# Kernel tuning notes

Hardware: AMD Instinct MI355X
Metric: run time of the kernel (lower is better)

## Reference

```python
import jax, jax.numpy as jnp
import numpy as np

B, C, T = 8, 512, 4096          # batch, channels (query/key/value/calc), time
NUM_HEADS = 8
HEAD_DIM = C // NUM_HEADS
EPS = 1e-6


def _rmsnorm(x, g):
    # x: [B, C, T], normalize over channel dim (num_features)
    return x * jax.lax.rsqrt(jnp.mean(x * x, axis=1, keepdims=True) + EPS) * g[None, :, None]


def _conv1x1(x, W, b):
    # pointwise Conv1d: W [out, in], x [B, in, T]
    return jnp.einsum('oc,bct->bot', W, x) + b[None, :, None]


def _feature(x, W, b, g):
    # Conv1d -> RMSNorm -> elu(x)+1
    return jax.nn.elu(_rmsnorm(_conv1x1(x, W, b), g)) + 1.0


def setup_inputs() -> dict:
    key = jax.random.key(0)
    ks = jax.random.split(key, 16)
    s = 1.0 / np.sqrt(C)
    inp = {
        'queries': jax.random.normal(ks[0], (B, C, T), dtype=jnp.float32),
        'keys': jax.random.normal(ks[1], (B, C, T), dtype=jnp.float32),
        'values': jax.random.normal(ks[2], (B, C, T), dtype=jnp.float32),
        'key_padding_masks': jax.random.randint(ks[3], (B, T), 0, 2).astype(bool),
        'Wq': jax.random.normal(ks[4], (C, C), dtype=jnp.float32) * s,
        'bq': jnp.zeros((C,), dtype=jnp.float32),
        'gq': jnp.ones((C,), dtype=jnp.float32),
        'Wk': jax.random.normal(ks[5], (C, C), dtype=jnp.float32) * s,
        'bk': jnp.zeros((C,), dtype=jnp.float32),
        'gk': jnp.ones((C,), dtype=jnp.float32),
        'Wv': jax.random.normal(ks[6], (C, C), dtype=jnp.float32) * s,
        'bv': jnp.zeros((C,), dtype=jnp.float32),
        'gv': jnp.ones((C,), dtype=jnp.float32),
        'Wp': jax.random.normal(ks[7], (C, C), dtype=jnp.float32) * s,
        'bp': jnp.zeros((C,), dtype=jnp.float32),
        'g_out': jnp.ones((C,), dtype=jnp.float32),
    }
    return inp


def reference(queries, keys, values, key_padding_masks,
              Wq, bq, gq, Wk, bk, gk, Wv, bv, gv, Wp, bp, g_out):
    residuals = queries
    q = _feature(queries, Wq, bq, gq)   # [B, C, Tq]
    k = _feature(keys, Wk, bk, gk)      # [B, C, Tk]
    v = _feature(values, Wv, bv, gv)    # [B, C, Tk]

    # split heads: (head dim) channel layout -> [B, H, Dh, T]
    q = q.reshape(B, NUM_HEADS, HEAD_DIM, -1)
    k = k.reshape(B, NUM_HEADS, HEAD_DIM, -1)
    v = v.reshape(B, NUM_HEADS, HEAD_DIM, -1)

    k = jnp.where(key_padding_masks[:, None, None, :], -10000.0, k)

    q = jax.nn.softmax(q, axis=2) * (NUM_HEADS ** -0.5)  # softmax over head_dim
    k = jax.nn.softmax(k, axis=3)                         # softmax over key time
    v = v / HEAD_DIM

    # linear attention: KV composition then QKV
    ctx = jnp.einsum('bhkt,bhvt->bhkv', k, v)             # [B, H, Dh, Dh]
    out = jnp.einsum('bhqt,bhqv->bhvt', q, ctx)           # [B, H, Dh, Tq]

    out = out.reshape(B, C, -1)
    out = _conv1x1(out, Wp, bp)
    return _rmsnorm(out + residuals, g_out)
```

## Files before the change

### kernel.cpp

```cpp
#include <hip/hip_runtime.h>
#include <hip/hip_bf16.h>

#define BB 8
#define CC 512
#define TT 4096
#define HH 8
#define DH 64
#define EPS 1e-6f

#define NROWS (BB * TT)

using bf16x8 = __attribute__((ext_vector_type(8))) short;
using s16x4  = __attribute__((ext_vector_type(4))) short;
using f32x4  = __attribute__((ext_vector_type(4))) float;

__device__ __forceinline__ short f2b(float f) {
  __hip_bfloat16 h = __float2bfloat16(f);
  return *reinterpret_cast<short*>(&h);
}
__device__ __forceinline__ float b2f(short s) {
  unsigned u = ((unsigned)(unsigned short)s) << 16;
  return __uint_as_float(u);
}

__device__ __forceinline__ void gld16(short* lds_dst, const short* gsrc) {
  __builtin_amdgcn_global_load_lds(
      (const __attribute__((address_space(1))) unsigned int*)gsrc,
      (__attribute__((address_space(3))) unsigned int*)lds_dst, 16, 0, 0);
}

__global__ __launch_bounds__(256) void conv_w4(const float* __restrict__ s0, const float* __restrict__ s1,
                                               const float* __restrict__ s2, const float* __restrict__ s3,
                                               short* __restrict__ d0, short* __restrict__ d1,
                                               short* __restrict__ d2, short* __restrict__ d3)
{
  const float* src; short* dst;
  switch (blockIdx.y) {
    case 0: src = s0; dst = d0; break;
    case 1: src = s1; dst = d1; break;
    case 2: src = s2; dst = d2; break;
    default: src = s3; dst = d3; break;
  }
  int i8 = (blockIdx.x * 256 + threadIdx.x) * 8;
  float4 a = *(const float4*)(src + i8);
  float4 b = *(const float4*)(src + i8 + 4);
  bf16x8 h = { f2b(a.x), f2b(a.y), f2b(a.z), f2b(a.w),
               f2b(b.x), f2b(b.y), f2b(b.z), f2b(b.w) };
  *(bf16x8*)(dst + i8) = h;
}

__global__ __launch_bounds__(256) void transpose_cvt3(const float* __restrict__ X0,
                                                      const float* __restrict__ X1,
                                                      const float* __restrict__ X2,
                                                      short* __restrict__ Y0,
                                                      short* __restrict__ Y1,
                                                      short* __restrict__ Y2)
{
  __shared__ short tile[64 * 68];
  const int t0 = blockIdx.x * 64, c0 = blockIdx.y * 64;
  const int b = blockIdx.z & 7, which = blockIdx.z >> 3;
  const float* X = which == 0 ? X0 : (which == 1 ? X1 : X2);
  short* Xt = which == 0 ? Y0 : (which == 1 ? Y1 : Y2);
  const int tid = threadIdx.x;
  {
    int cl = tid >> 4, t4 = (tid & 15) * 4;
    #pragma unroll
    for (int it = 0; it < 4; ++it) {
      int c = it * 16 + cl;
      float4 v = *(const float4*)(X + ((size_t)b * CC + c0 + c) * TT + t0 + t4);
      s16x4 h = { f2b(v.x), f2b(v.y), f2b(v.z), f2b(v.w) };
      *(s16x4*)&tile[c * 68 + t4] = h;
    }
  }
  __syncthreads();
  {
    int t = tid >> 2, ci = (tid & 3) * 16;
    short s[16];
    #pragma unroll
    for (int i = 0; i < 16; ++i) s[i] = tile[(ci + i) * 68 + t];
    short* dst = Xt + ((size_t)b * TT + t0 + t) * CC + c0 + ci;
    *(bf16x8*)dst = *(bf16x8*)&s[0];
    *(bf16x8*)(dst + 8) = *(bf16x8*)&s[8];
  }
}

__global__ __launch_bounds__(256) void gemm_tc(const short* __restrict__ A,
                                               const short* __restrict__ W,
                                               const float* __restrict__ bias,
                                               short* __restrict__ Y)
{
  __shared__ short As[2][4096];
  __shared__ short Bs[2][4096];
  const int tid = threadIdx.x;
  int x = blockIdx.x;
  int wg = (x & 7) * 128 + (x >> 3);
  const int m0 = (wg >> 2) * 128;
  const int o0 = (wg & 3) * 128;

  const int wid = tid >> 6, lane = tid & 63;
  const int wr = (wid >> 1) * 64, wc = (wid & 1) * 64;
  const int lr = lane & 15, g = lane >> 4;
  const int swz8 = (g ^ ((lr >> 1) & 3)) * 8;

  const int srow0 = tid >> 2;
  const int scol  = ((tid & 3) ^ ((tid >> 3) & 3)) * 8;

  f32x4 acc[4][4] = {};

  #pragma unroll
  for (int it = 0; it < 2; ++it) {
    int row = it * 64 + srow0;
    gld16(&As[0][it * 2048 + tid * 8], A + (size_t)(m0 + row) * CC + scol);
    gld16(&Bs[0][it * 2048 + tid * 8], W + (size_t)(o0 + row) * CC + scol);
  }
  __syncthreads();

  for (int step = 0; step < 16; ++step) {
    const int cur = step & 1;
    if (step < 15) {
      const int k0 = (step + 1) * 32;
      #pragma unroll
      for (int it = 0; it < 2; ++it) {
        int row = it * 64 + srow0;
        gld16(&As[cur ^ 1][it * 2048 + tid * 8], A + (size_t)(m0 + row) * CC + k0 + scol);
        gld16(&Bs[cur ^ 1][it * 2048 + tid * 8], W + (size_t)(o0 + row) * CC + k0 + scol);
      }
    }
    bf16x8 af[4], bf[4];
    #pragma unroll
    for (int m = 0; m < 4; ++m) af[m] = *(const bf16x8*)&As[cur][(wr + m * 16 + lr) * 32 + swz8];
    #pragma unroll
    for (int n = 0; n < 4; ++n) bf[n] = *(const bf16x8*)&Bs[cur][(wc + n * 16 + lr) * 32 + swz8];
    #pragma unroll
    for (int m = 0; m < 4; ++m)
      #pragma unroll
      for (int n = 0; n < 4; ++n)
        acc[m][n] = __builtin_amdgcn_mfma_f32_16x16x32_bf16(af[m], bf[n], acc[m][n], 0, 0, 0);
    __syncthreads();
  }

  const int lq4 = (lane >> 4) * 4;
  #pragma unroll
  for (int m = 0; m < 4; ++m)
    #pragma unroll
    for (int r = 0; r < 4; ++r) {
      size_t row = (size_t)(m0 + wr + m * 16 + lq4 + r) * CC;
      #pragma unroll
      for (int n = 0; n < 4; ++n) {
        int o = o0 + wc + n * 16 + lr;
        Y[row + o] = f2b(acc[m][n][r] + bias[o]);
      }
    }
}

template<int MODE>
__global__ __launch_bounds__(256) void feat_row(short* __restrict__ buf,
                                                const float* __restrict__ g,
                                                const unsigned char* __restrict__ mask)
{
  const int row = blockIdx.x * 4 + (threadIdx.x >> 6);
  const int lane = threadIdx.x & 63;
  short* p = buf + (size_t)row * CC + lane * 8;
  if constexpr (MODE == 1) {
    if (mask[row]) {
      bf16x8 z = { 0,0,0,0,0,0,0,0 };
      *(bf16x8*)p = z;
      return;
    }
  }
  bf16x8 v = *(const bf16x8*)p;
  float x[8], ss = 0.f;
  #pragma unroll
  for (int j = 0; j < 8; ++j) { x[j] = b2f(v[j]); ss += x[j] * x[j]; }
  #pragma unroll
  for (int off = 32; off; off >>= 1) ss += __shfl_xor(ss, off);
  float rn = rsqrtf(ss * (1.0f / CC) + EPS);
  float4 g0 = *(const float4*)(g + lane * 8);
  float4 g1 = *(const float4*)(g + lane * 8 + 4);
  float gv[8] = { g0.x, g0.y, g0.z, g0.w, g1.x, g1.y, g1.z, g1.w };
  float f[8];
  #pragma unroll
  for (int j = 0; j < 8; ++j) {
    float t = x[j] * rn * gv[j];
    f[j] = t > 0.f ? t + 1.f : __expf(t);
  }
  bf16x8 o;
  if constexpr (MODE == 1) {
    #pragma unroll
    for (int j = 0; j < 8; ++j) o[j] = f2b(__expf(f[j]));
  } else if constexpr (MODE == 2) {
    #pragma unroll
    for (int j = 0; j < 8; ++j) o[j] = f2b(f[j] * (1.0f / DH));
  } else {
    float ls = 0.f;
    #pragma unroll
    for (int j = 0; j < 8; ++j) { f[j] = __expf(f[j]); ls += f[j]; }
    ls += __shfl_xor(ls, 1); ls += __shfl_xor(ls, 2); ls += __shfl_xor(ls, 4);
    float sc = 0.35355339059327373f / ls;
    #pragma unroll
    for (int j = 0; j < 8; ++j) o[j] = f2b(f[j] * sc);
  }
  *(bf16x8*)p = o;
}

__global__ __launch_bounds__(256) void ksm_sum(const short* __restrict__ kfe,
                                               float* __restrict__ S)
{
  const int b = blockIdx.y, tch = blockIdx.x;
  const int c2 = threadIdx.x * 2;
  float s0 = 0.f, s1 = 0.f;
  for (int t = 0; t < 128; ++t) {
    unsigned u = *(const unsigned*)&kfe[((size_t)b * TT + tch * 128 + t) * CC + c2];
    s0 += __uint_as_float(u << 16);
    s1 += __uint_as_float(u & 0xffff0000u);
  }
  atomicAdd(&S[b * CC + c2], s0);
  atomicAdd(&S[b * CC + c2 + 1], s1);
}

__global__ __launch_bounds__(256) void ctx_t(const short* __restrict__ kf,
                                             const short* __restrict__ vf,
                                             float* __restrict__ P)
{
  __shared__ short Ks[64 * 64];
  __shared__ short Vs[64 * 64];
  const int tc = blockIdx.x, bh = blockIdx.y;
  const int b = bh >> 3, h = bh & 7;
  const int tid = threadIdx.x, wid = tid >> 6, lane = tid & 63;
  const int lr = lane & 15, lg = lane >> 4;
  f32x4 acc[4] = {};

  for (int ts = 0; ts < 8; ++ts) {
    #pragma unroll
    for (int i = 0; i < 2; ++i) {
      int n = i * 256 + tid;
      int t = n >> 3, ch = (n & 7) * 8;
      size_t src = ((size_t)b * TT + tc * 512 + ts * 64 + t) * CC + h * DH + ch;
      gld16(Ks + n * 8, kf + src);
      gld16(Vs + n * 8, vf + src);
    }
    __syncthreads();
    #pragma unroll
    for (int kk = 0; kk < 64; kk += 32) {
      short a[8];
      #pragma unroll
      for (int j = 0; j < 8; ++j)
        a[j] = Ks[(kk + lg * 8 + j) * 64 + wid * 16 + lr];
      bf16x8 af = *(const bf16x8*)&a[0];
      #pragma unroll
      for (int n = 0; n < 4; ++n) {
        short bv[8];
        #pragma unroll
        for (int j = 0; j < 8; ++j)
          bv[j] = Vs[(kk + lg * 8 + j) * 64 + n * 16 + lr];
        acc[n] = __builtin_amdgcn_mfma_f32_16x16x32_bf16(af, *(const bf16x8*)&bv[0],
                                                         acc[n], 0, 0, 0);
      }
    }
    __syncthreads();
  }
  float* pp = P + ((size_t)tc * 64 + bh) * (DH * DH);
  const int lq4 = lg * 4;
  #pragma unroll
  for (int n = 0; n < 4; ++n)
    #pragma unroll
    for (int r = 0; r < 4; ++r)
      pp[(wid * 16 + lq4 + r) * DH + n * 16 + lr] = acc[n][r];
}

__global__ __launch_bounds__(256) void ctx_reduce(const float* __restrict__ P,
                                                  const float* __restrict__ S,
                                                  short* __restrict__ CT)
{
  int i = blockIdx.x * 256 + threadIdx.x;
  float s = 0.f;
  #pragma unroll
  for (int c = 0; c < 8; ++c) s += P[(size_t)c * 64 * DH * DH + i];
  int bh = i >> 12, rem = i & 4095, q = rem >> 6, v = rem & 63;
  int b = bh >> 3, h = bh & 7;
  float inv = 1.f / S[b * CC + h * DH + q];
  CT[((size_t)bh << 12) + v * 64 + q] = f2b(s * inv);
}

__global__ __launch_bounds__(256) void attn_t(const short* __restrict__ qf,
                                              const short* __restrict__ CT,
                                              short* __restrict__ ao)
{
  __shared__ short As[128 * 72];
  __shared__ short Cs[64 * 72];
  const int m0 = blockIdx.x * 128, h = blockIdx.y;
  const int tid = threadIdx.x, wid = tid >> 6, lane = tid & 63;
  const int lr = lane & 15, lk8 = (lane >> 4) * 8;

  #pragma unroll
  for (int i = 0; i < 4; ++i) {
    int n = i * 256 + tid;
    int r = n >> 3, ch = (n & 7) * 8;
    *(bf16x8*)&As[r * 72 + ch] =
        *(const bf16x8*)(qf + (size_t)(m0 + r) * CC + h * DH + ch);
  }
  {
    const int bh0 = (m0 / TT) * 8 + h;
    #pragma unroll
    for (int i = 0; i < 2; ++i) {
      int n = i * 256 + tid;
      int v = n >> 3, ch = (n & 7) * 8;
      *(bf16x8*)&Cs[v * 72 + ch] = *(const bf16x8*)(CT + ((size_t)bh0 << 12) + v * 64 + ch);
    }
  }
  __syncthreads();

  const int wr = wid * 32;
  f32x4 acc[2][4] = {};
  #pragma unroll
  for (int kk = 0; kk < 64; kk += 32) {
    bf16x8 af[2], cf[4];
    #pragma unroll
    for (int m = 0; m < 2; ++m) af[m] = *(const bf16x8*)&As[(wr + m * 16 + lr) * 72 + kk + lk8];
    #pragma unroll
    for (int n = 0; n < 4; ++n) cf[n] = *(const bf16x8*)&Cs[(n * 16 + lr) * 72 + kk + lk8];
    #pragma unroll
    for (int m = 0; m < 2; ++m)
      #pragma unroll
      for (int n = 0; n < 4; ++n)
        acc[m][n] = __builtin_amdgcn_mfma_f32_16x16x32_bf16(af[m], cf[n], acc[m][n], 0, 0, 0);
  }
  const int lq4 = (lane >> 4) * 4;
  #pragma unroll
  for (int m = 0; m < 2; ++m)
    #pragma unroll
    for (int r = 0; r < 4; ++r) {
      size_t row = (size_t)(m0 + wr + m * 16 + lq4 + r) * CC + h * DH;
      #pragma unroll
      for (int n = 0; n < 4; ++n)
        ao[row + n * 16 + lr] = f2b(acc[m][n][r]);
    }
}

__global__ __launch_bounds__(256) void final_fused(const short* __restrict__ pj,
                                                   const short* __restrict__ qt,
                                                   const float* __restrict__ g,
                                                   float* __restrict__ out)
{
  __shared__ float tile[64 * 65];
  __shared__ float rmss[64];
  const int t0 = blockIdx.x * 64, b = blockIdx.y;
  const int tid = threadIdx.x;

  {
    const int t = tid >> 2, cb = (tid & 3) * 128;
    const size_t row = ((size_t)b * TT + t0 + t) * CC + cb;
    float ss = 0.f;
    #pragma unroll
    for (int j = 0; j < 16; ++j) {
      bf16x8 a = *(const bf16x8*)(pj + row + j * 8);
      bf16x8 q = *(const bf16x8*)(qt + row + j * 8);
      #pragma unroll
      for (int e = 0; e < 8; ++e) { float z = b2f(a[e]) + b2f(q[e]); ss += z * z; }
    }
    ss += __shfl_xor(ss, 1);
    ss += __shfl_xor(ss, 2);
    if ((tid & 3) == 0) rmss[t] = rsqrtf(ss * (1.0f / CC) + EPS);
  }
  __syncthreads();

  for (int cb8 = 0; cb8 < 8; ++cb8) {
    const int c0 = cb8 * 64;
    {
      const int t = tid >> 2, ch = (tid & 3) * 16;
      const size_t row = ((size_t)b * TT + t0 + t) * CC + c0 + ch;
      bf16x8 a0 = *(const bf16x8*)(pj + row);
      bf16x8 a1 = *(const bf16x8*)(pj + row + 8);
      bf16x8 q0 = *(const bf16x8*)(qt + row);
      bf16x8 q1 = *(const bf16x8*)(qt + row + 8);
      const float r = rmss[t];
      #pragma unroll
      for (int j = 0; j < 8; ++j) {
        tile[(ch + j) * 65 + t]     = (b2f(a0[j]) + b2f(q0[j])) * r * g[c0 + ch + j];
        tile[(ch + 8 + j) * 65 + t] = (b2f(a1[j]) + b2f(q1[j])) * r * g[c0 + ch + 8 + j];
      }
    }
    __syncthreads();
    {
      const int c = tid >> 2, tc = (tid & 3) * 16;
      float* dst = out + ((size_t)b * CC + c0 + c) * TT + t0 + tc;
      #pragma unroll
      for (int i = 0; i < 4; ++i) {
        float4 v = { tile[c * 65 + tc + i * 4],     tile[c * 65 + tc + i * 4 + 1],
                     tile[c * 65 + tc + i * 4 + 2], tile[c * 65 + tc + i * 4 + 3] };
        *(float4*)(dst + i * 4) = v;
      }
    }
    __syncthreads();
  }
}

extern "C" void kernel_launch(void* const* d_in, const int* in_sizes, int n_in,
                              void* d_out, int out_size, void* d_ws, size_t ws_size,
                              hipStream_t stream) {
  (void)in_sizes; (void)n_in; (void)out_size; (void)ws_size;
  const float* queries = (const float*)d_in[0];
  const float* keys    = (const float*)d_in[1];
  const float* values  = (const float*)d_in[2];
  const unsigned char* mask = (const unsigned char*)d_in[3];
  const float* Wq = (const float*)d_in[4];
  const float* bq = (const float*)d_in[5];
  const float* gq = (const float*)d_in[6];
  const float* Wk = (const float*)d_in[7];
  const float* bk = (const float*)d_in[8];
  const float* gk = (const float*)d_in[9];
  const float* Wv = (const float*)d_in[10];
  const float* bv = (const float*)d_in[11];
  const float* gv = (const float*)d_in[12];
  const float* Wp = (const float*)d_in[13];
  const float* bp = (const float*)d_in[14];
  const float* g_out = (const float*)d_in[15];

  const size_t NCT = (size_t)NROWS * CC;
  short* qt = (short*)d_ws;
  short* kt = qt + NCT;
  short* vt = kt + NCT;
  short* qf = vt + NCT;
  short* kf = qf + NCT;
  short* vf = kf + NCT;
  short* ao = kt;
  short* pj = vt;
  float* ctxP = (float*)(vf + NCT);
  short* CT  = (short*)(ctxP + (size_t)8 * 64 * DH * DH);
  short* wqb = CT + (size_t)64 * DH * DH;
  short* wkb = wqb + (size_t)CC * CC;
  short* wvb = wkb + (size_t)CC * CC;
  short* wpb = wvb + (size_t)CC * CC;
  float* S   = (float*)(wpb + (size_t)CC * CC);

  hipMemsetAsync(S, 0, (size_t)BB * CC * sizeof(float), stream);

  conv_w4<<<dim3(CC * CC / 2048, 4), 256, 0, stream>>>(Wq, Wk, Wv, Wp, wqb, wkb, wvb, wpb);

  transpose_cvt3<<<dim3(TT / 64, CC / 64, 3 * BB), 256, 0, stream>>>(
      queries, keys, values, qt, kt, vt);

  dim3 gG(1024);
  gemm_tc<<<gG, 256, 0, stream>>>(qt, wqb, bq, qf);
  gemm_tc<<<gG, 256, 0, stream>>>(kt, wkb, bk, kf);
  gemm_tc<<<gG, 256, 0, stream>>>(vt, wvb, bv, vf);

  feat_row<0><<<dim3(NROWS / 4), 256, 0, stream>>>(qf, gq, mask);
  feat_row<1><<<dim3(NROWS / 4), 256, 0, stream>>>(kf, gk, mask);
  feat_row<2><<<dim3(NROWS / 4), 256, 0, stream>>>(vf, gv, mask);

  ksm_sum<<<dim3(32, BB), 256, 0, stream>>>(kf, S);

  ctx_t<<<dim3(8, BB * HH), 256, 0, stream>>>(kf, vf, ctxP);
  ctx_reduce<<<dim3(64 * DH * DH / 256), 256, 0, stream>>>(ctxP, S, CT);

  attn_t<<<dim3(NROWS / 128, HH), 256, 0, stream>>>(qf, CT, ao);

  gemm_tc<<<gG, 256, 0, stream>>>(ao, wpb, bp, pj);

  final_fused<<<dim3(TT / 64, BB), 256, 0, stream>>>(pj, qt, g_out, (float*)d_out);
}
```

Before: 339.9 us.

## Batch QKV GEMMs and feature kernels, pipeline transpose, cache residual in LDS

Merges the three QKV projection GEMMs and the three feature-normalization kernels into single launches indexed by blockIdx.y. The transpose kernel now processes four 64-wide time tiles per block, prefetching the next tile into registers while double-buffering LDS. The final RMSNorm kernel keeps the bf16 residual sum in a large LDS buffer so the projection and residual are read from global memory only once. This trades launch count and global traffic for much higher LDS use per block, which lowers occupancy, and adds bf16 rounding of the residual sum before the final scale.

```diff
diff --git a/kernel.cpp b/kernel.cpp
--- a/kernel.cpp
+++ b/kernel.cpp
@@ -56,32 +56,124 @@
                                                       short* __restrict__ Y1,
                                                       short* __restrict__ Y2)
 {
-  __shared__ short tile[64 * 68];
-  const int t0 = blockIdx.x * 64, c0 = blockIdx.y * 64;
+  __shared__ short tile[2][64 * 68];
+  const int t0 = blockIdx.x * 256, c0 = blockIdx.y * 64;
   const int b = blockIdx.z & 7, which = blockIdx.z >> 3;
   const float* X = which == 0 ? X0 : (which == 1 ? X1 : X2);
   short* Xt = which == 0 ? Y0 : (which == 1 ? Y1 : Y2);
   const int tid = threadIdx.x;
-  {
-    int cl = tid >> 4, t4 = (tid & 15) * 4;
+  const int cl = tid >> 4, t4 = (tid & 15) * 4;
+  const int tb = tid >> 2, ci = (tid & 3) * 16;
+
+  float4 r[4];
+  #pragma unroll
+  for (int it = 0; it < 4; ++it)
+    r[it] = *(const float4*)(X + ((size_t)b * CC + c0 + it * 16 + cl) * TT + t0 + t4);
+
+  for (int s = 0; s < 4; ++s) {
+    const int cur = s & 1;
     #pragma unroll
     for (int it = 0; it < 4; ++it) {
-      int c = it * 16 + cl;
-      float4 v = *(const float4*)(X + ((size_t)b * CC + c0 + c) * TT + t0 + t4);
-      s16x4 h = { f2b(v.x), f2b(v.y), f2b(v.z), f2b(v.w) };
-      *(s16x4*)&tile[c * 68 + t4] = h;
-    }
+      s16x4 h = { f2b(r[it].x), f2b(r[it].y), f2b(r[it].z), f2b(r[it].w) };
+      *(s16x4*)&tile[cur][(it * 16 + cl) * 68 + t4] = h;
+    }
+    if (s < 3) {
+      #pragma unroll
+      for (int it = 0; it < 4; ++it)
+        r[it] = *(const float4*)(X + ((size_t)b * CC + c0 + it * 16 + cl) * TT
+                                 + t0 + (s + 1) * 64 + t4);
+    }
+    __syncthreads();
+    short sreg[16];
+    #pragma unroll
+    for (int i = 0; i < 16; ++i) sreg[i] = tile[cur][(ci + i) * 68 + tb];
+    short* dst = Xt + ((size_t)b * TT + t0 + s * 64 + tb) * CC + c0 + ci;
+    *(bf16x8*)dst = *(bf16x8*)&sreg[0];
+    *(bf16x8*)(dst + 8) = *(bf16x8*)&sreg[8];
+  }
+}
+
+__device__ __forceinline__ void gemm_body(const short* __restrict__ A,
+                                          const short* __restrict__ W,
+                                          const float* __restrict__ bias,
+                                          short* __restrict__ Y,
+                                          short* As, short* Bs, int x, int tid)
+{
+  int wg = (x & 7) * 128 + (x >> 3);
+  const int m0 = (wg >> 2) * 128;
+  const int o0 = (wg & 3) * 128;
+
+  const int wid = tid >> 6, lane = tid & 63;
+  const int wr = (wid >> 1) * 64, wc = (wid & 1) * 64;
+  const int lr = lane & 15, g = lane >> 4;
+  const int swz8 = (g ^ ((lr >> 1) & 3)) * 8;
+
+  const int srow0 = tid >> 2;
+  const int scol  = ((tid & 3) ^ ((tid >> 3) & 3)) * 8;
+
+  f32x4 acc[4][4] = {};
+
+  #pragma unroll
+  for (int it = 0; it < 2; ++it) {
+    int row = it * 64 + srow0;
+    gld16(&As[it * 2048 + tid * 8], A + (size_t)(m0 + row) * CC + scol);
+    gld16(&Bs[it * 2048 + tid * 8], W + (size_t)(o0 + row) * CC + scol);
   }
   __syncthreads();
-  {
-    int t = tid >> 2, ci = (tid & 3) * 16;
-    short s[16];
-    #pragma unroll
-    for (int i = 0; i < 16; ++i) s[i] = tile[(ci + i) * 68 + t];
-    short* dst = Xt + ((size_t)b * TT + t0 + t) * CC + c0 + ci;
-    *(bf16x8*)dst = *(bf16x8*)&s[0];
-    *(bf16x8*)(dst + 8) = *(bf16x8*)&s[8];
-  }
+
+  for (int step = 0; step < 16; ++step) {
+    const int cur = step & 1;
+    if (step < 15) {
+      const int k0 = (step + 1) * 32;
+      #pragma unroll
+      for (int it = 0; it < 2; ++it) {
+        int row = it * 64 + srow0;
+        gld16(&As[(cur ^ 1) * 4096 + it * 2048 + tid * 8], A + (size_t)(m0 + row) * CC + k0 + scol);
+        gld16(&Bs[(cur ^ 1) * 4096 + it * 2048 + tid * 8], W + (size_t)(o0 + row) * CC + k0 + scol);
+      }
+    }
+    bf16x8 af[4], bf[4];
+    #pragma unroll
+    for (int m = 0; m < 4; ++m) af[m] = *(const bf16x8*)&As[cur * 4096 + (wr + m * 16 + lr) * 32 + swz8];
+    #pragma unroll
+    for (int n = 0; n < 4; ++n) bf[n] = *(const bf16x8*)&Bs[cur * 4096 + (wc + n * 16 + lr) * 32 + swz8];
+    #pragma unroll
+    for (int m = 0; m < 4; ++m)
+      #pragma unroll
+      for (int n = 0; n < 4; ++n)
+        acc[m][n] = __builtin_amdgcn_mfma_f32_16x16x32_bf16(af[m], bf[n], acc[m][n], 0, 0, 0);
+    __syncthreads();
+  }
+
+  const int lq4 = (lane >> 4) * 4;
+  #pragma unroll
+  for (int m = 0; m < 4; ++m)
+    #pragma unroll
+    for (int r = 0; r < 4; ++r) {
+      size_t row = (size_t)(m0 + wr + m * 16 + lq4 + r) * CC;
+      #pragma unroll
+      for (int n = 0; n < 4; ++n) {
+        int o = o0 + wc + n * 16 + lr;
+        Y[row + o] = f2b(acc[m][n][r] + bias[o]);
+      }
+    }
+}
+
+__global__ __launch_bounds__(256) void gemm_tc3(
+    const short* __restrict__ A0, const short* __restrict__ A1, const short* __restrict__ A2,
+    const short* __restrict__ W0, const short* __restrict__ W1, const short* __restrict__ W2,
+    const float* __restrict__ b0, const float* __restrict__ b1, const float* __restrict__ b2,
+    short* __restrict__ Y0, short* __restrict__ Y1, short* __restrict__ Y2)
+{
+  __shared__ short As[2 * 4096];
+  __shared__ short Bs[2 * 4096];
+  const short *A, *W; const float* bias; short* Y;
+  switch (blockIdx.y) {
+    case 0:  A = A0; W = W0; bias = b0; Y = Y0; break;
+    case 1:  A = A1; W = W1; bias = b1; Y = Y1; break;
+    default: A = A2; W = W2; bias = b2; Y = Y2; break;
+  }
+  gemm_body(A, W, bias, Y, As, Bs, blockIdx.x, threadIdx.x);
 }
 
 __global__ __launch_bounds__(256) void gemm_tc(const short* __restrict__ A,
@@ -89,84 +181,28 @@
                                                const float* __restrict__ bias,
                                                short* __restrict__ Y)
 {
-  __shared__ short As[2][4096];
-  __shared__ short Bs[2][4096];
-  const int tid = threadIdx.x;
-  int x = blockIdx.x;
-  int wg = (x & 7) * 128 + (x >> 3);
-  const int m0 = (wg >> 2) * 128;
-  const int o0 = (wg & 3) * 128;
-
-  const int wid = tid >> 6, lane = tid & 63;
-  const int wr = (wid >> 1) * 64, wc = (wid & 1) * 64;
-  const int lr = lane & 15, g = lane >> 4;
-  const int swz8 = (g ^ ((lr >> 1) & 3)) * 8;
-
-  const int srow0 = tid >> 2;
-  const int scol  = ((tid & 3) ^ ((tid >> 3) & 3)) * 8;
-
-  f32x4 acc[4][4] = {};
-
-  #pragma unroll
-  for (int it = 0; it < 2; ++it) {
-    int row = it * 64 + srow0;
-    gld16(&As[0][it * 2048 + tid * 8], A + (size_t)(m0 + row) * CC + scol);
-    gld16(&Bs[0][it * 2048 + tid * 8], W + (size_t)(o0 + row) * CC + scol);
-  }
-  __syncthreads();
-
-  for (int step = 0; step < 16; ++step) {
-    const int cur = step & 1;
-    if (step < 15) {
-      const int k0 = (step + 1) * 32;
-      #pragma unroll
-      for (int it = 0; it < 2; ++it) {
-        int row = it * 64 + srow0;
-        gld16(&As[cur ^ 1][it * 2048 + tid * 8], A + (size_t)(m0 + row) * CC + k0 + scol);
-        gld16(&Bs[cur ^ 1][it * 2048 + tid * 8], W + (size_t)(o0 + row) * CC + k0 + scol);
-      }
-    }
-    bf16x8 af[4], bf[4];
-    #pragma unroll
-    for (int m = 0; m < 4; ++m) af[m] = *(const bf16x8*)&As[cur][(wr + m * 16 + lr) * 32 + swz8];
-    #pragma unroll
-    for (int n = 0; n < 4; ++n) bf[n] = *(const bf16x8*)&Bs[cur][(wc + n * 16 + lr) * 32 + swz8];
-    #pragma unroll
-    for (int m = 0; m < 4; ++m)
-      #pragma unroll
-      for (int n = 0; n < 4; ++n)
-        acc[m][n] = __builtin_amdgcn_mfma_f32_16x16x32_bf16(af[m], bf[n], acc[m][n], 0, 0, 0);
-    __syncthreads();
-  }
-
-  const int lq4 = (lane >> 4) * 4;
-  #pragma unroll
-  for (int m = 0; m < 4; ++m)
-    #pragma unroll
-    for (int r = 0; r < 4; ++r) {
-      size_t row = (size_t)(m0 + wr + m * 16 + lq4 + r) * CC;
-      #pragma unroll
-      for (int n = 0; n < 4; ++n) {
-        int o = o0 + wc + n * 16 + lr;
-        Y[row + o] = f2b(acc[m][n][r] + bias[o]);
-      }
-    }
-}
-
-template<int MODE>
-__global__ __launch_bounds__(256) void feat_row(short* __restrict__ buf,
-                                                const float* __restrict__ g,
+  __shared__ short As[2 * 4096];
+  __shared__ short Bs[2 * 4096];
+  gemm_body(A, W, bias, Y, As, Bs, blockIdx.x, threadIdx.x);
+}
+
+__global__ __launch_bounds__(256) void feat_all(short* __restrict__ qf, short* __restrict__ kf,
+                                                short* __restrict__ vf,
+                                                const float* __restrict__ gq,
+                                                const float* __restrict__ gk,
+                                                const float* __restrict__ gv,
                                                 const unsigned char* __restrict__ mask)
 {
+  const int mode = blockIdx.y;
+  short* buf = mode == 0 ? qf : (mode == 1 ? kf : vf);
+  const float* g = mode == 0 ? gq : (mode == 1 ? gk : gv);
   const int row = blockIdx.x * 4 + (threadIdx.x >> 6);
   const int lane = threadIdx.x & 63;
   short* p = buf + (size_t)row * CC + lane * 8;
-  if constexpr (MODE == 1) {
-    if (mask[row]) {
-      bf16x8 z = { 0,0,0,0,0,0,0,0 };
-      *(bf16x8*)p = z;
-      return;
-    }
+  if (mode == 1 && mask[row]) {
+    bf16x8 z = { 0,0,0,0,0,0,0,0 };
+    *(bf16x8*)p = z;
+    return;
   }
   bf16x8 v = *(const bf16x8*)p;
   float x[8], ss = 0.f;
@@ -177,18 +213,18 @@
   float rn = rsqrtf(ss * (1.0f / CC) + EPS);
   float4 g0 = *(const float4*)(g + lane * 8);
   float4 g1 = *(const float4*)(g + lane * 8 + 4);
-  float gv[8] = { g0.x, g0.y, g0.z, g0.w, g1.x, g1.y, g1.z, g1.w };
+  float gv8[8] = { g0.x, g0.y, g0.z, g0.w, g1.x, g1.y, g1.z, g1.w };
   float f[8];
   #pragma unroll
   for (int j = 0; j < 8; ++j) {
-    float t = x[j] * rn * gv[j];
+    float t = x[j] * rn * gv8[j];
     f[j] = t > 0.f ? t + 1.f : __expf(t);
   }
   bf16x8 o;
-  if constexpr (MODE == 1) {
+  if (mode == 1) {
     #pragma unroll
     for (int j = 0; j < 8; ++j) o[j] = f2b(__expf(f[j]));
-  } else if constexpr (MODE == 2) {
+  } else if (mode == 2) {
     #pragma unroll
     for (int j = 0; j < 8; ++j) o[j] = f2b(f[j] * (1.0f / DH));
   } else {
@@ -342,7 +378,7 @@
                                                    const float* __restrict__ g,
                                                    float* __restrict__ out)
 {
-  __shared__ float tile[64 * 65];
+  __shared__ short z[512 * 72];
   __shared__ float rmss[64];
   const int t0 = blockIdx.x * 64, b = blockIdx.y;
   const int tid = threadIdx.x;
@@ -356,7 +392,11 @@
       bf16x8 a = *(const bf16x8*)(pj + row + j * 8);
       bf16x8 q = *(const bf16x8*)(qt + row + j * 8);
       #pragma unroll
-      for (int e = 0; e < 8; ++e) { float z = b2f(a[e]) + b2f(q[e]); ss += z * z; }
+      for (int e = 0; e < 8; ++e) {
+        float zf = b2f(a[e]) + b2f(q[e]);
+        ss += zf * zf;
+        z[(cb + j * 8 + e) * 72 + t] = f2b(zf);
+      }
     }
     ss += __shfl_xor(ss, 1);
     ss += __shfl_xor(ss, 2);
@@ -364,34 +404,26 @@
   }
   __syncthreads();
 
+  const int c = tid >> 2, tcs = (tid & 3) * 16;
+  #pragma unroll 1
   for (int cb8 = 0; cb8 < 8; ++cb8) {
-    const int c0 = cb8 * 64;
-    {
-      const int t = tid >> 2, ch = (tid & 3) * 16;
-      const size_t row = ((size_t)b * TT + t0 + t) * CC + c0 + ch;
-      bf16x8 a0 = *(const bf16x8*)(pj + row);
-      bf16x8 a1 = *(const bf16x8*)(pj + row + 8);
-      bf16x8 q0 = *(const bf16x8*)(qt + row);
-      bf16x8 q1 = *(const bf16x8*)(qt + row + 8);
-      const float r = rmss[t];
-      #pragma unroll
-      for (int j = 0; j < 8; ++j) {
-        tile[(ch + j) * 65 + t]     = (b2f(a0[j]) + b2f(q0[j])) * r * g[c0 + ch + j];
-        tile[(ch + 8 + j) * 65 + t] = (b2f(a1[j]) + b2f(q1[j])) * r * g[c0 + ch + 8 + j];
-      }
-    }
-    __syncthreads();
-    {
-      const int c = tid >> 2, tc = (tid & 3) * 16;
-      float* dst = out + ((size_t)b * CC + c0 + c) * TT + t0 + tc;
-      #pragma unroll
-      for (int i = 0; i < 4; ++i) {
-        float4 v = { tile[c * 65 + tc + i * 4],     tile[c * 65 + tc + i * 4 + 1],
-                     tile[c * 65 + tc + i * 4 + 2], tile[c * 65 + tc + i * 4 + 3] };
-        *(float4*)(dst + i * 4) = v;
-      }
-    }
-    __syncthreads();
+    const int cc = cb8 * 64 + c;
+    const float gc = g[cc];
+    bf16x8 z0 = *(const bf16x8*)&z[cc * 72 + tcs];
+    bf16x8 z1 = *(const bf16x8*)&z[cc * 72 + tcs + 8];
+    float* dst = out + ((size_t)b * CC + cc) * TT + t0 + tcs;
+    #pragma unroll
+    for (int i = 0; i < 2; ++i) {
+      float4 o0 = { b2f(z0[i*4+0]) * rmss[tcs+i*4+0] * gc, b2f(z0[i*4+1]) * rmss[tcs+i*4+1] * gc,
+                    b2f(z0[i*4+2]) * rmss[tcs+i*4+2] * gc, b2f(z0[i*4+3]) * rmss[tcs+i*4+3] * gc };
+      *(float4*)(dst + i * 4) = o0;
+    }
+    #pragma unroll
+    for (int i = 0; i < 2; ++i) {
+      float4 o1 = { b2f(z1[i*4+0]) * rmss[tcs+8+i*4+0] * gc, b2f(z1[i*4+1]) * rmss[tcs+8+i*4+1] * gc,
+                    b2f(z1[i*4+2]) * rmss[tcs+8+i*4+2] * gc, b2f(z1[i*4+3]) * rmss[tcs+8+i*4+3] * gc };
+      *(float4*)(dst + 8 + i * 4) = o1;
+    }
   }
 }
 
@@ -437,17 +469,13 @@
 
   conv_w4<<<dim3(CC * CC / 2048, 4), 256, 0, stream>>>(Wq, Wk, Wv, Wp, wqb, wkb, wvb, wpb);
 
-  transpose_cvt3<<<dim3(TT / 64, CC / 64, 3 * BB), 256, 0, stream>>>(
+  transpose_cvt3<<<dim3(TT / 256, CC / 64, 3 * BB), 256, 0, stream>>>(
       queries, keys, values, qt, kt, vt);
 
-  dim3 gG(1024);
-  gemm_tc<<<gG, 256, 0, stream>>>(qt, wqb, bq, qf);
-  gemm_tc<<<gG, 256, 0, stream>>>(kt, wkb, bk, kf);
-  gemm_tc<<<gG, 256, 0, stream>>>(vt, wvb, bv, vf);
-
-  feat_row<0><<<dim3(NROWS / 4), 256, 0, stream>>>(qf, gq, mask);
-  feat_row<1><<<dim3(NROWS / 4), 256, 0, stream>>>(kf, gk, mask);
-  feat_row<2><<<dim3(NROWS / 4), 256, 0, stream>>>(vf, gv, mask);
+  gemm_tc3<<<dim3(1024, 3), 256, 0, stream>>>(qt, kt, vt, wqb, wkb, wvb,
+                                              bq, bk, bv, qf, kf, vf);
+
+  feat_all<<<dim3(NROWS / 4, 3), 256, 0, stream>>>(qf, kf, vf, gq, gk, gv, mask);
 
   ksm_sum<<<dim3(32, BB), 256, 0, stream>>>(kf, S);
 
@@ -456,7 +484,7 @@
 
   attn_t<<<dim3(NROWS / 128, HH), 256, 0, stream>>>(qf, CT, ao);
 
-  gemm_tc<<<gG, 256, 0, stream>>>(ao, wpb, bp, pj);
+  gemm_tc<<<dim3(1024), 256, 0, stream>>>(ao, wpb, bp, pj);
 
   final_fused<<<dim3(TT / 64, BB), 256, 0, stream>>>(pj, qt, g_out, (float*)d_out);
 }
```

Result: faster. 319.3 us (-6.0%).
